# Optimization experiments

Measured on AMD Instinct MI355X. Metric: run time of the kernel, lower is better.

The kernel has to match this reference:

```python
import jax, jax.numpy as jnp
import numpy as np

B, S, D = 2, 2048, 2048          # batch, seq_len, model_dim
H, HD, RD, L = 16, 128, 64, 512  # heads, head_dim, rope_dim, latent_dim


def _rope_cos_sin(seq_len, dim, dtype):
    inv_freq = 1.0 / (10000.0 ** (jnp.arange(0, dim, 2, dtype=jnp.float32) / dim))
    freqs = jnp.outer(jnp.arange(seq_len, dtype=jnp.float32), inv_freq)  # [S, dim/2]
    emb = jnp.concatenate([freqs, freqs], axis=-1)                        # [S, dim]
    return jnp.cos(emb).astype(dtype), jnp.sin(emb).astype(dtype)


def _rotate_half(x):
    x1, x2 = jnp.split(x, 2, axis=-1)
    return jnp.concatenate([-x2, x1], axis=-1)


def _apply_rope(q, k):
    # q, k: [B, S, H, rope_dim]
    cos, sin = _rope_cos_sin(q.shape[1], q.shape[-1], q.dtype)
    cos = cos[None, :, None, :]
    sin = sin[None, :, None, :]
    return q * cos + _rotate_half(q) * sin, k * cos + _rotate_half(k) * sin


def setup_inputs() -> dict:
    key = jax.random.key(0)
    ks = jax.random.split(key, 6)
    x = jax.random.normal(ks[0], (B, S, D), dtype=jnp.float32)
    mask = jnp.tril(jnp.ones((1, 1, S, S), dtype=jnp.bool_))  # causal
    s = lambda fan_in: 1.0 / np.sqrt(fan_in)
    w_kv_down = jax.random.normal(ks[1], (D, L), jnp.float32) * s(D)
    w_kv_up = jax.random.normal(ks[2], (L, H * (2 * HD + RD)), jnp.float32) * s(L)
    w_q_down = jax.random.normal(ks[3], (D, L), jnp.float32) * s(D)
    w_q_up = jax.random.normal(ks[4], (L, H * (HD + RD)), jnp.float32) * s(L)
    w_o = jax.random.normal(ks[5], (H * HD, D), jnp.float32) * s(H * HD)
    return dict(x=x, mask=mask, w_kv_down=w_kv_down, w_kv_up=w_kv_up,
                w_q_down=w_q_down, w_q_up=w_q_up, w_o=w_o)


def reference(x, mask, w_kv_down, w_kv_up, w_q_down, w_q_up, w_o):
    b, s, _ = x.shape
    # low-rank KV path
    kv_full = (x @ w_kv_down @ w_kv_up).reshape(b, s, H, 2 * HD + RD)
    k_content = kv_full[..., :HD]
    k_rope = kv_full[..., HD:HD + RD]
    v = kv_full[..., HD + RD:]                     # [b, s, H, HD]
    # low-rank Q path
    q_full = (x @ w_q_down @ w_q_up).reshape(b, s, H, HD + RD)
    q_content = q_full[..., :HD]
    q_rope = q_full[..., HD:]
    # partial RoPE on the rope slice only
    q_rope, k_rope = _apply_rope(q_rope, k_rope)
    q = jnp.concatenate([q_content, q_rope], axis=-1)  # [b, s, H, HD+RD]
    k = jnp.concatenate([k_content, k_rope], axis=-1)
    scale = 1.0 / np.sqrt(HD + RD)
    scores = jnp.einsum('bqhd,bkhd->bhqk', q, k) * scale
    scores = jnp.where(mask, scores, jnp.finfo(scores.dtype).min)
    attn = jax.nn.softmax(scores, axis=-1)          # dropout_p=0.0 -> identity
    context = jnp.einsum('bhqk,bkhd->bqhd', attn, v).reshape(b, s, H * HD)
    return context @ w_o
```

## Files before the change

### kernel.cpp

```cpp
#include <hip/hip_runtime.h>
#include <hip/hip_bf16.h>

#define B_ 2
#define S_ 2048
#define D_ 2048
#define H_ 16
#define HD_ 128
#define RD_ 64
#define L_ 512
#define BS_ (B_ * S_)
#define KVH 320
#define QH 192

typedef unsigned short u16;
typedef __bf16 bf16x8 __attribute__((ext_vector_type(8)));
typedef float f32x4 __attribute__((ext_vector_type(4)));
typedef float f32x16 __attribute__((ext_vector_type(16)));
typedef unsigned short us8 __attribute__((ext_vector_type(8)));
typedef unsigned short us4 __attribute__((ext_vector_type(4)));

#define MFMA16(A, B, C) __builtin_amdgcn_mfma_f32_16x16x32_bf16((A), (B), (C), 0, 0, 0)
#define MFMA32(A, B, C) __builtin_amdgcn_mfma_f32_32x32x16_bf16((A), (B), (C), 0, 0, 0)

__device__ __forceinline__ u16 f2bf(float f) {
    unsigned int u = __builtin_bit_cast(unsigned int, f);
    u += 0x7FFFu + ((u >> 16) & 1u);
    return (u16)(u >> 16);
}
__device__ __forceinline__ float bf2f(u16 u) {
    unsigned int x = ((unsigned int)u) << 16;
    return __builtin_bit_cast(float, x);
}
__device__ __forceinline__ void async16(const void* g, void* l) {
    __builtin_amdgcn_global_load_lds((void __attribute__((address_space(1)))*)g,
                                     (void __attribute__((address_space(3)))*)l, 16, 0, 0);
}
__device__ __forceinline__ int swz4(int row) { return (row + (row >> 2)) & 3; }
__device__ __forceinline__ unsigned int cvtpk_bf16(float lo, float hi) {
    unsigned int r;
    asm("v_cvt_pk_bf16_f32 %0, %1, %2" : "=v"(r) : "v"(lo), "v"(hi));
    return r;
}

__global__ __launch_bounds__(256) void conv_f32_bf16(const float* __restrict__ in,
                                                     u16* __restrict__ outp) {
    const int i = blockIdx.x * 256 + threadIdx.x;
    float4 v = *(const float4*)(in + (size_t)i * 4);
    us4 o; o[0] = f2bf(v.x); o[1] = f2bf(v.y); o[2] = f2bf(v.z); o[3] = f2bf(v.w);
    *(us4*)(outp + (size_t)i * 4) = o;
}

__global__ __launch_bounds__(256) void transpose_f32_bf16(const float* __restrict__ W,
                                                          u16* __restrict__ Wt,
                                                          int K, int N) {
    __shared__ float tile[32][33];
    const int t = threadIdx.x, tx = t & 31, ty = t >> 5;
    const int n0 = blockIdx.x * 32, k0 = blockIdx.y * 32;
#pragma unroll
    for (int r = 0; r < 4; r++)
        tile[ty + 8 * r][tx] = W[(size_t)(k0 + ty + 8 * r) * N + n0 + tx];
    __syncthreads();
#pragma unroll
    for (int r = 0; r < 4; r++)
        Wt[(size_t)(n0 + ty + 8 * r) * K + k0 + tx] = f2bf(tile[tx][ty + 8 * r]);
}

__global__ __launch_bounds__(256) void transpose_v(const u16* __restrict__ kvf,
                                                   u16* __restrict__ vtg) {
    __shared__ u16 tile[32][33];
    const int t = threadIdx.x, tx = t & 31, ty = t >> 5;
    const int bh = blockIdx.z, b = bh >> 4, h = bh & 15;
    const int s0 = blockIdx.x * 32, d0 = blockIdx.y * 32;
#pragma unroll
    for (int r = 0; r < 4; r++)
        tile[ty + 8 * r][tx] = kvf[(size_t)(b * S_ + s0 + ty + 8 * r) * (H_ * KVH) + h * KVH + QH + d0 + tx];
    __syncthreads();
#pragma unroll
    for (int r = 0; r < 4; r++)
        vtg[((size_t)bh * HD_ + d0 + ty + 8 * r) * S_ + s0 + tx] = tile[tx][ty + 8 * r];
}

__global__ __launch_bounds__(256) void rope_both(u16* __restrict__ qf,
                                                 u16* __restrict__ kvf) {
    const int idx = blockIdx.x * 256 + threadIdx.x;
    const int d = idx & 31;
    const int h = (idx >> 5) & (H_ - 1);
    const int s = (idx >> 9) & (S_ - 1);
    const int b = idx >> 20;
    const int stride = blockIdx.y ? KVH : QH;
    u16* buf = blockIdx.y ? kvf : qf;

    const float inv_freq = powf(10000.0f, -(float)d * (1.0f / 32.0f));
    const float ang = (float)s * inv_freq;
    const float c = cosf(ang), sn = sinf(ang);

    u16* p = buf + ((size_t)((b * S_ + s) * H_) + h) * stride + HD_ + d;
    const float x1 = bf2f(p[0]);
    const float x2 = bf2f(p[32]);
    p[0]  = f2bf(x1 * c - x2 * sn);
    p[32] = f2bf(x2 * c + x1 * sn);
}

template <int WM, int WN, int TM, int TN, bool OUT_F32>
__global__ __launch_bounds__(WM * WN * 64) void gemm_bf16(
    const u16* __restrict__ A, int lda,
    const u16* __restrict__ Bt, int ldb,
    void* __restrict__ Cv, int ldc, int K) {
    constexpr int BMt = WM * TM * 16;
    constexpr int BNt = WN * TN * 16;
    constexpr int NW  = WM * WN;
    constexpr int CA  = BMt / 16;
    constexpr int CB  = BNt / 16;

    __shared__ u16 As[BMt * 32];
    __shared__ u16 Bs[BNt * 32];

    const int t = threadIdx.x, w = t >> 6, l = t & 63;
    const int quad = l >> 4, n16 = l & 15;
    const int wr = w / WN, wc = w % WN;
    const size_t m0 = (size_t)blockIdx.y * BMt;
    const size_t n0 = (size_t)blockIdx.x * BNt;
    const int rowc = l >> 2, sbp = l & 3;

    f32x4 acc[TM][TN];
#pragma unroll
    for (int i = 0; i < TM; i++)
#pragma unroll
        for (int j = 0; j < TN; j++) acc[i][j] = (f32x4){0.f, 0.f, 0.f, 0.f};

    for (int k0 = 0; k0 < K; k0 += 32) {
#pragma unroll
        for (int c = w; c < CA; c += NW) {
            const int row = c * 16 + rowc;
            const int colc = ((sbp - swz4(row)) & 3) * 8;
            async16(A + (m0 + row) * lda + k0 + colc, &As[c * 512 + l * 8]);
        }
#pragma unroll
        for (int c = w; c < CB; c += NW) {
            const int row = c * 16 + rowc;
            const int colc = ((sbp - swz4(row)) & 3) * 8;
            async16(Bt + (n0 + row) * ldb + k0 + colc, &Bs[c * 512 + l * 8]);
        }
        __syncthreads();

        bf16x8 af[TM], bfr[TN];
#pragma unroll
        for (int i = 0; i < TM; i++) {
            const int row = wr * TM * 16 + i * 16 + n16;
            af[i] = *(const bf16x8*)&As[row * 32 + ((quad + swz4(row)) & 3) * 8];
        }
#pragma unroll
        for (int j = 0; j < TN; j++) {
            const int row = wc * TN * 16 + j * 16 + n16;
            bfr[j] = *(const bf16x8*)&Bs[row * 32 + ((quad + swz4(row)) & 3) * 8];
        }
#pragma unroll
        for (int i = 0; i < TM; i++)
#pragma unroll
            for (int j = 0; j < TN; j++) acc[i][j] = MFMA16(af[i], bfr[j], acc[i][j]);
        __syncthreads();
    }

#pragma unroll
    for (int i = 0; i < TM; i++) {
#pragma unroll
        for (int j = 0; j < TN; j++) {
#pragma unroll
            for (int r = 0; r < 4; r++) {
                const size_t row = m0 + wr * TM * 16 + i * 16 + quad * 4 + r;
                const size_t col = n0 + wc * TN * 16 + j * 16 + n16;
                if (OUT_F32) ((float*)Cv)[row * ldc + col] = acc[i][j][r];
                else         ((u16*)Cv)[row * ldc + col] = f2bf(acc[i][j][r]);
            }
        }
    }
}

__global__ __launch_bounds__(256, 2) void attn_mfma(const u16* __restrict__ qf,
                                                    const u16* __restrict__ kvf,
                                                    const u16* __restrict__ vtg,
                                                    u16* __restrict__ ctx) {
    __shared__ u16 Ks[2][3 * 64 * 64];
    __shared__ u16 Vs[128 * 64];

    const int t = threadIdx.x, w = t >> 6, lane = t & 63;
    const int l31 = lane & 31, hi = lane >> 5;

    const int wg = blockIdx.x;
    const int xcd = wg & 7, ii = wg >> 3;
    const int tt = ii & 15;
    const int pp = (tt & 1) ? (tt >> 1) : (15 - (tt >> 1));
    const int qi = (ii & 32) ? (15 - pp) : pp;
    const int bh = xcd + 8 * (ii >> 4);
    const int b = bh >> 4, h = bh & 15;
    const int Q0 = qi * 128;

    const float sc2 = 1.442695041f / 13.856406461f;

    const u16* Kbase = kvf + (size_t)(b * S_) * (H_ * KVH) + h * KVH;
    const u16* Vbase = vtg + (size_t)bh * HD_ * S_;

    const int scol = ((lane & 7) ^ (lane >> 3)) * 8;
    const int krl  = lane >> 3;

    bf16x8 qfrag[12];
    {
        const u16* qr = qf + (size_t)(b * S_ + Q0 + w * 32 + l31) * (H_ * QH) + h * QH + hi * 8;
#pragma unroll
        for (int c = 0; c < 12; c++) qfrag[c] = *(const bf16x8*)(qr + c * 16);
    }
    asm volatile("" ::: "memory");

    f32x16 O[4];
#pragma unroll
    for (int i = 0; i < 4; i++)
#pragma unroll
        for (int r = 0; r < 16; r++) O[i][r] = 0.f;
    float lrun = 0.f;

    const int qg = Q0 + w * 32 + l31;
    const int qmaxw = Q0 + w * 32 + 31;
    const int nkt = Q0 / 64 + 2;

#define ISSUE_K(KT, BUF)                                                        \
    _Pragma("unroll")                                                           \
    for (int ch = w; ch < 24; ch += 4) {                                        \
        const int c3 = ch >> 3, kq = ch & 7;                                    \
        async16(Kbase + (size_t)((KT) * 64 + kq * 8 + krl) * (H_ * KVH)         \
                      + c3 * 64 + scol,                                         \
                &Ks[BUF][c3 * 4096 + kq * 512 + lane * 8]);                     \
    }
#define ISSUE_V(KT)                                                             \
    _Pragma("unroll")                                                           \
    for (int ch = w; ch < 16; ch += 4) {                                        \
        async16(Vbase + (size_t)(ch * 8 + krl) * S_ + (KT) * 64 + scol,         \
                &Vs[ch * 512 + lane * 8]);                                      \
    }

    ISSUE_K(0, 0);
    ISSUE_V(0);

    for (int kt = 0; kt < nkt; kt++) {
        const int cur = kt & 1;
        if (kt > 0) {
            asm volatile("s_barrier" ::: "memory");
            ISSUE_V(kt);
        }
        if (kt + 1 < nkt) {
            ISSUE_K(kt + 1, cur ^ 1);
            asm volatile("s_waitcnt vmcnt(10)" ::: "memory");
        } else {
            asm volatile("s_waitcnt vmcnt(4)" ::: "memory");
        }
        asm volatile("s_barrier" ::: "memory");

        const bool active = (kt * 64) <= qmaxw;
        bf16x8 pfrag[4];
        if (active) {
            const int swz = (l31 & 7) * 8;
            f32x16 sA, sB;
#pragma unroll
            for (int r = 0; r < 16; r++) { sA[r] = 0.f; sB[r] = 0.f; }
            __builtin_amdgcn_s_setprio(1);
#pragma unroll
            for (int c = 0; c < 12; c++) {
                const int cb = (c & 3) * 16 + hi * 8;
                const int base = (c >> 2) * 4096 + (cb ^ swz);
                bf16x8 kf0 = *(const bf16x8*)&Ks[cur][base + l31 * 64];
                bf16x8 kf1 = *(const bf16x8*)&Ks[cur][base + (32 + l31) * 64];
                sA = MFMA32(kf0, qfrag[c], sA);
                sB = MFMA32(kf1, qfrag[c], sB);
            }
            __builtin_amdgcn_s_setprio(0);

            const bool diag = (kt * 64 + 63) > (Q0 + w * 32);
#pragma unroll
            for (int r = 0; r < 16; r++) {
                const int crow = (r & 3) + 8 * (r >> 2) + 4 * hi;
                float pa = exp2f(sA[r] * sc2);
                float pb = exp2f(sB[r] * sc2);
                if (diag) {
                    if (kt * 64 + crow > qg) pa = 0.f;
                    if (kt * 64 + 32 + crow > qg) pb = 0.f;
                }
                lrun += pa + pb;
                sA[r] = pa;
                sB[r] = pb;
            }

#pragma unroll
            for (int s = 0; s < 4; s++) {
                const f32x16 src = (s < 2) ? sA : sB;
                const int r0 = (s & 1) * 8;
                unsigned int x0 = cvtpk_bf16(src[r0 + 0], src[r0 + 1]);
                unsigned int y0 = cvtpk_bf16(src[r0 + 4], src[r0 + 5]);
                unsigned int x1 = cvtpk_bf16(src[r0 + 2], src[r0 + 3]);
                unsigned int y1 = cvtpk_bf16(src[r0 + 6], src[r0 + 7]);
                asm volatile("v_permlane32_swap_b32 %0, %1" : "+v"(x0), "+v"(y0));
                asm volatile("v_permlane32_swap_b32 %0, %1" : "+v"(x1), "+v"(y1));
                union { unsigned int wv[4]; bf16x8 v; } u;
                u.wv[0] = x0; u.wv[1] = x1; u.wv[2] = y0; u.wv[3] = y1;
                pfrag[s] = u.v;
            }
        }

        if (kt + 1 < nkt) asm volatile("s_waitcnt vmcnt(6)" ::: "memory");
        else              asm volatile("s_waitcnt vmcnt(0)" ::: "memory");
        asm volatile("s_barrier" ::: "memory");

        if (active) {
            __builtin_amdgcn_s_setprio(1);
#pragma unroll
            for (int s = 0; s < 4; s++) {
#pragma unroll
                for (int dt = 0; dt < 4; dt++) {
                    const int d = dt * 32 + l31;
                    bf16x8 vf = *(const bf16x8*)&Vs[d * 64 + ((s * 16 + hi * 8) ^ ((d & 7) * 8))];
                    O[dt] = MFMA32(pfrag[s], vf, O[dt]);
                }
            }
            __builtin_amdgcn_s_setprio(0);
        }
    }
#undef ISSUE_K
#undef ISSUE_V

    lrun += __shfl_xor(lrun, 32, 64);
    float inv[16];
#pragma unroll
    for (int r = 0; r < 16; r++) {
        const int crow = (r & 3) + 8 * (r >> 2) + 4 * hi;
        inv[r] = 1.0f / __shfl(lrun, crow, 64);
    }
#pragma unroll
    for (int dt = 0; dt < 4; dt++)
#pragma unroll
        for (int r = 0; r < 16; r++) {
            const int crow = (r & 3) + 8 * (r >> 2) + 4 * hi;
            const int qrow = Q0 + w * 32 + crow;
            ctx[(size_t)(b * S_ + qrow) * (H_ * HD_) + h * HD_ + dt * 32 + l31] =
                f2bf(O[dt][r] * inv[r]);
        }
}

extern "C" void kernel_launch(void* const* d_in, const int* in_sizes, int n_in,
                              void* d_out, int out_size, void* d_ws, size_t ws_size,
                              hipStream_t stream) {
    const float* x         = (const float*)d_in[0];
    const float* w_kv_down = (const float*)d_in[2];
    const float* w_kv_up   = (const float*)d_in[3];
    const float* w_q_down  = (const float*)d_in[4];
    const float* w_q_up    = (const float*)d_in[5];
    const float* w_o       = (const float*)d_in[6];
    float* out = (float*)d_out;

    char* ws = (char*)d_ws;
    size_t off = 0;
    u16* xb      = (u16*)(ws + off); off += (size_t)BS_ * D_ * 2;
    u16* wdt     = (u16*)(ws + off); off += (size_t)1024 * D_ * 2;
    u16* wkvup_t = (u16*)(ws + off); off += (size_t)(H_ * KVH) * L_ * 2;
    u16* wqup_t  = (u16*)(ws + off); off += (size_t)(H_ * QH) * L_ * 2;
    u16* wo_t    = (u16*)(ws + off); off += (size_t)D_ * (H_ * HD_) * 2;
    u16* low     = (u16*)(ws + off); off += (size_t)BS_ * 1024 * 2;
    u16* kv_full = (u16*)(ws + off); off += (size_t)BS_ * H_ * KVH * 2;
    u16* q_full  = (u16*)(ws + off); off += (size_t)BS_ * H_ * QH * 2;
    u16* vtg     = (u16*)(ws + off); off += (size_t)B_ * H_ * HD_ * S_ * 2;
    u16* ctx     = (u16*)(ws + off); off += (size_t)BS_ * H_ * HD_ * 2;

    conv_f32_bf16<<<(BS_ * D_) / 1024, 256, 0, stream>>>(x, xb);
    transpose_f32_bf16<<<dim3(L_ / 32, D_ / 32), 256, 0, stream>>>(w_kv_down, wdt, D_, L_);
    transpose_f32_bf16<<<dim3(L_ / 32, D_ / 32), 256, 0, stream>>>(w_q_down, wdt + (size_t)512 * D_, D_, L_);
    transpose_f32_bf16<<<dim3((H_ * KVH) / 32, L_ / 32), 256, 0, stream>>>(w_kv_up, wkvup_t, L_, H_ * KVH);
    transpose_f32_bf16<<<dim3((H_ * QH) / 32, L_ / 32), 256, 0, stream>>>(w_q_up, wqup_t, L_, H_ * QH);
    transpose_f32_bf16<<<dim3(D_ / 32, (H_ * HD_) / 32), 256, 0, stream>>>(w_o, wo_t, H_ * HD_, D_);

    gemm_bf16<2, 2, 4, 2, false><<<dim3(1024 / 64, BS_ / 128), 256, 0, stream>>>(
        xb, D_, wdt, D_, low, 1024, D_);
    gemm_bf16<2, 2, 4, 4, false><<<dim3((H_ * KVH) / 128, BS_ / 128), 256, 0, stream>>>(
        low, 1024, wkvup_t, L_, kv_full, H_ * KVH, L_);
    gemm_bf16<2, 2, 4, 4, false><<<dim3((H_ * QH) / 128, BS_ / 128), 256, 0, stream>>>(
        low + 512, 1024, wqup_t, L_, q_full, H_ * QH, L_);

    rope_both<<<dim3((B_ * S_ * H_ * 32) / 256, 2), 256, 0, stream>>>(q_full, kv_full);

    transpose_v<<<dim3(S_ / 32, HD_ / 32, B_ * H_), 256, 0, stream>>>(kv_full, vtg);

    attn_mfma<<<dim3(512), 256, 0, stream>>>(q_full, kv_full, vtg, ctx);

    gemm_bf16<2, 2, 4, 4, true><<<dim3(D_ / 128, BS_ / 128), 256, 0, stream>>>(
        ctx, D_, wo_t, D_, out, D_, D_);
}
```

Measured before the change: 399.3 us.

## Software-pipeline attention QK and softmax-PV across tiles, pair causal query blocks per workgroup

The attention kernel is restructured so the QK^T MFMAs for the next key tile overlap the exp/PV work of the previous tile, using a triple-buffered V tile in LDS and precomputed swizzled LDS offsets. Each workgroup now processes a complementary pair of query blocks (qi and 15-qi) sequentially, giving it a constant amount of causal work, so the grid is halved and occupancy is set to one block per CU. The softmax scale times log2(e) is folded into the Q-projection GEMM epilogue through a new alpha parameter, which removes the per-element multiply in attention. The trade-offs are more LDS and register pressure, fewer resident waves, and Q being rounded to bf16 after scaling.

```diff
diff --git a/kernel.cpp b/kernel.cpp
--- a/kernel.cpp
+++ b/kernel.cpp
@@ -105,7 +105,7 @@
 __global__ __launch_bounds__(WM * WN * 64) void gemm_bf16(
     const u16* __restrict__ A, int lda,
     const u16* __restrict__ Bt, int ldb,
-    void* __restrict__ Cv, int ldc, int K) {
+    void* __restrict__ Cv, int ldc, int K, float alpha) {
     constexpr int BMt = WM * TM * 16;
     constexpr int BNt = WN * TN * 16;
     constexpr int NW  = WM * WN;
@@ -169,33 +169,29 @@
             for (int r = 0; r < 4; r++) {
                 const size_t row = m0 + wr * TM * 16 + i * 16 + quad * 4 + r;
                 const size_t col = n0 + wc * TN * 16 + j * 16 + n16;
-                if (OUT_F32) ((float*)Cv)[row * ldc + col] = acc[i][j][r];
-                else         ((u16*)Cv)[row * ldc + col] = f2bf(acc[i][j][r]);
+                const float v = acc[i][j][r] * alpha;
+                if (OUT_F32) ((float*)Cv)[row * ldc + col] = v;
+                else         ((u16*)Cv)[row * ldc + col] = f2bf(v);
             }
         }
     }
 }
 
-__global__ __launch_bounds__(256, 2) void attn_mfma(const u16* __restrict__ qf,
+__global__ __launch_bounds__(256, 1) void attn_mfma(const u16* __restrict__ qf,
                                                     const u16* __restrict__ kvf,
                                                     const u16* __restrict__ vtg,
                                                     u16* __restrict__ ctx) {
     __shared__ u16 Ks[2][3 * 64 * 64];
-    __shared__ u16 Vs[128 * 64];
+    __shared__ u16 Vs[3][128 * 64];
 
     const int t = threadIdx.x, w = t >> 6, lane = t & 63;
     const int l31 = lane & 31, hi = lane >> 5;
 
     const int wg = blockIdx.x;
-    const int xcd = wg & 7, ii = wg >> 3;
-    const int tt = ii & 15;
-    const int pp = (tt & 1) ? (tt >> 1) : (15 - (tt >> 1));
-    const int qi = (ii & 32) ? (15 - pp) : pp;
-    const int bh = xcd + 8 * (ii >> 4);
+    const int xcd = wg & 7, j = wg >> 3;
+    const int bh = xcd + 8 * (j & 3);
+    const int qpair = j >> 2;
     const int b = bh >> 4, h = bh & 15;
-    const int Q0 = qi * 128;
-
-    const float sc2 = 1.442695041f / 13.856406461f;
 
     const u16* Kbase = kvf + (size_t)(b * S_) * (H_ * KVH) + h * KVH;
     const u16* Vbase = vtg + (size_t)bh * HD_ * S_;
@@ -203,24 +199,16 @@
     const int scol = ((lane & 7) ^ (lane >> 3)) * 8;
     const int krl  = lane >> 3;
 
-    bf16x8 qfrag[12];
-    {
-        const u16* qr = qf + (size_t)(b * S_ + Q0 + w * 32 + l31) * (H_ * QH) + h * QH + hi * 8;
-#pragma unroll
-        for (int c = 0; c < 12; c++) qfrag[c] = *(const bf16x8*)(qr + c * 16);
-    }
-    asm volatile("" ::: "memory");
-
-    f32x16 O[4];
-#pragma unroll
-    for (int i = 0; i < 4; i++)
-#pragma unroll
-        for (int r = 0; r < 16; r++) O[i][r] = 0.f;
-    float lrun = 0.f;
-
-    const int qg = Q0 + w * 32 + l31;
-    const int qmaxw = Q0 + w * 32 + 31;
-    const int nkt = Q0 / 64 + 2;
+    int koff[12];
+#pragma unroll
+    for (int c = 0; c < 12; c++)
+        koff[c] = (c >> 2) * 4096 + (((c & 3) * 16 + hi * 8) ^ ((l31 & 7) * 8));
+    int voff[4][4];
+#pragma unroll
+    for (int s = 0; s < 4; s++)
+#pragma unroll
+        for (int dt = 0; dt < 4; dt++)
+            voff[s][dt] = (dt * 32 + l31) * 64 + ((s * 16 + hi * 8) ^ ((l31 & 7) * 8));
 
 #define ISSUE_K(KT, BUF)                                                        \
     _Pragma("unroll")                                                           \
@@ -230,117 +218,147 @@
                       + c3 * 64 + scol,                                         \
                 &Ks[BUF][c3 * 4096 + kq * 512 + lane * 8]);                     \
     }
-#define ISSUE_V(KT)                                                             \
+#define ISSUE_V(KT, VB)                                                         \
     _Pragma("unroll")                                                           \
     for (int ch = w; ch < 16; ch += 4) {                                        \
         async16(Vbase + (size_t)(ch * 8 + krl) * S_ + (KT) * 64 + scol,         \
-                &Vs[ch * 512 + lane * 8]);                                      \
-    }
-
-    ISSUE_K(0, 0);
-    ISSUE_V(0);
-
-    for (int kt = 0; kt < nkt; kt++) {
-        const int cur = kt & 1;
-        if (kt > 0) {
+                &Vs[VB][ch * 512 + lane * 8]);                                  \
+    }
+
+#define QK_TILE(TILE, SA, SB)                                                   \
+    {                                                                           \
+        const int kb_ = (TILE) & 1;                                             \
+        _Pragma("unroll")                                                       \
+        for (int r = 0; r < 16; r++) { SA[r] = 0.f; SB[r] = 0.f; }              \
+        _Pragma("unroll")                                                       \
+        for (int c = 0; c < 12; c++) {                                          \
+            bf16x8 kf0 = *(const bf16x8*)&Ks[kb_][koff[c] + l31 * 64];          \
+            bf16x8 kf1 = *(const bf16x8*)&Ks[kb_][koff[c] + (32 + l31) * 64];   \
+            SA = MFMA32(kf0, qfrag[c], SA);                                     \
+            SB = MFMA32(kf1, qfrag[c], SB);                                     \
+        }                                                                       \
+    }
+
+#define SMPV_TILE(TILE, SA, SB)                                                 \
+    {                                                                           \
+        const int vb_ = (TILE) % 3;                                             \
+        const bool diag_ = ((TILE) * 64 + 63) > (Q0 + w * 32);                  \
+        _Pragma("unroll")                                                       \
+        for (int r = 0; r < 16; r++) {                                          \
+            float pa = exp2f(SA[r]);                                            \
+            float pb = exp2f(SB[r]);                                            \
+            if (diag_) {                                                        \
+                const int crow_ = (r & 3) + 8 * (r >> 2) + 4 * hi;              \
+                if ((TILE) * 64 + crow_ > qg) pa = 0.f;                         \
+                if ((TILE) * 64 + 32 + crow_ > qg) pb = 0.f;                    \
+            }                                                                   \
+            lrun += pa + pb;                                                    \
+            SA[r] = pa; SB[r] = pb;                                             \
+        }                                                                       \
+        bf16x8 pfrag[4];                                                        \
+        _Pragma("unroll")                                                       \
+        for (int s = 0; s < 4; s++) {                                           \
+            const int r0 = (s & 1) * 8;                                         \
+            unsigned int x0, y0, x1, y1;                                        \
+            if (s < 2) {                                                        \
+                x0 = cvtpk_bf16(SA[r0 + 0], SA[r0 + 1]);                        \
+                y0 = cvtpk_bf16(SA[r0 + 4], SA[r0 + 5]);                        \
+                x1 = cvtpk_bf16(SA[r0 + 2], SA[r0 + 3]);                        \
+                y1 = cvtpk_bf16(SA[r0 + 6], SA[r0 + 7]);                        \
+            } else {                                                            \
+                x0 = cvtpk_bf16(SB[r0 + 0], SB[r0 + 1]);                        \
+                y0 = cvtpk_bf16(SB[r0 + 4], SB[r0 + 5]);                        \
+                x1 = cvtpk_bf16(SB[r0 + 2], SB[r0 + 3]);                        \
+                y1 = cvtpk_bf16(SB[r0 + 6], SB[r0 + 7]);                        \
+            }                                                                   \
+            asm volatile("v_permlane32_swap_b32 %0, %1" : "+v"(x0), "+v"(y0));  \
+            asm volatile("v_permlane32_swap_b32 %0, %1" : "+v"(x1), "+v"(y1));  \
+            union { unsigned int wv[4]; bf16x8 v; } u_;                         \
+            u_.wv[0] = x0; u_.wv[1] = x1; u_.wv[2] = y0; u_.wv[3] = y1;         \
+            pfrag[s] = u_.v;                                                    \
+        }                                                                       \
+        _Pragma("unroll")                                                       \
+        for (int s = 0; s < 4; s++) {                                           \
+            _Pragma("unroll")                                                   \
+            for (int dt = 0; dt < 4; dt++) {                                    \
+                bf16x8 vf = *(const bf16x8*)&Vs[vb_][voff[s][dt]];              \
+                O[dt] = MFMA32(pfrag[s], vf, O[dt]);                            \
+            }                                                                   \
+        }                                                                       \
+    }
+
+#pragma unroll 1
+    for (int half = 0; half < 2; half++) {
+        const int qi = half ? (15 - qpair) : qpair;
+        const int Q0 = qi * 128;
+        const int nkt = 2 * qi + 2;
+        const int qmaxw = Q0 + w * 32 + 31;
+        const int qg = Q0 + w * 32 + l31;
+
+        asm volatile("s_barrier" ::: "memory");
+
+        bf16x8 qfrag[12];
+        {
+            const u16* qr = qf + (size_t)(b * S_ + Q0 + w * 32 + l31) * (H_ * QH) + h * QH + hi * 8;
+#pragma unroll
+            for (int c = 0; c < 12; c++) qfrag[c] = *(const bf16x8*)(qr + c * 16);
+        }
+        asm volatile("" ::: "memory");
+
+        f32x16 O[4];
+#pragma unroll
+        for (int i = 0; i < 4; i++)
+#pragma unroll
+            for (int r = 0; r < 16; r++) O[i][r] = 0.f;
+        float lrun = 0.f;
+        f32x16 sEa, sEb, sOa, sOb;
+
+        ISSUE_K(0, 0);
+        ISSUE_V(0, 0);
+
+        for (int kt = 0; kt < nkt; kt += 2) {
+            ISSUE_K(kt + 1, (kt + 1) & 1);
+            ISSUE_V(kt + 1, (kt + 1) % 3);
+            asm volatile("s_waitcnt vmcnt(10)" ::: "memory");
             asm volatile("s_barrier" ::: "memory");
-            ISSUE_V(kt);
-        }
-        if (kt + 1 < nkt) {
-            ISSUE_K(kt + 1, cur ^ 1);
-            asm volatile("s_waitcnt vmcnt(10)" ::: "memory");
-        } else {
-            asm volatile("s_waitcnt vmcnt(4)" ::: "memory");
-        }
-        asm volatile("s_barrier" ::: "memory");
-
-        const bool active = (kt * 64) <= qmaxw;
-        bf16x8 pfrag[4];
-        if (active) {
-            const int swz = (l31 & 7) * 8;
-            f32x16 sA, sB;
-#pragma unroll
-            for (int r = 0; r < 16; r++) { sA[r] = 0.f; sB[r] = 0.f; }
-            __builtin_amdgcn_s_setprio(1);
-#pragma unroll
-            for (int c = 0; c < 12; c++) {
-                const int cb = (c & 3) * 16 + hi * 8;
-                const int base = (c >> 2) * 4096 + (cb ^ swz);
-                bf16x8 kf0 = *(const bf16x8*)&Ks[cur][base + l31 * 64];
-                bf16x8 kf1 = *(const bf16x8*)&Ks[cur][base + (32 + l31) * 64];
-                sA = MFMA32(kf0, qfrag[c], sA);
-                sB = MFMA32(kf1, qfrag[c], sB);
+            QK_TILE(kt, sEa, sEb);
+            if (kt > 0) SMPV_TILE(kt - 1, sOa, sOb);
+            asm volatile("s_barrier" ::: "memory");
+            if (kt + 2 < nkt) {
+                ISSUE_K(kt + 2, kt & 1);
+                ISSUE_V(kt + 2, (kt + 2) % 3);
+                asm volatile("s_waitcnt vmcnt(10)" ::: "memory");
+            } else {
+                asm volatile("s_waitcnt vmcnt(0)" ::: "memory");
             }
-            __builtin_amdgcn_s_setprio(0);
-
-            const bool diag = (kt * 64 + 63) > (Q0 + w * 32);
+            asm volatile("s_barrier" ::: "memory");
+            if ((kt + 1) * 64 <= qmaxw) QK_TILE(kt + 1, sOa, sOb);
+            SMPV_TILE(kt, sEa, sEb);
+            asm volatile("s_barrier" ::: "memory");
+        }
+        if ((nkt - 1) * 64 <= qmaxw) SMPV_TILE(nkt - 1, sOa, sOb);
+
+        lrun += __shfl_xor(lrun, 32, 64);
+        float inv_[16];
+#pragma unroll
+        for (int r = 0; r < 16; r++) {
+            const int crow = (r & 3) + 8 * (r >> 2) + 4 * hi;
+            inv_[r] = 1.0f / __shfl(lrun, crow, 64);
+        }
+#pragma unroll
+        for (int dt = 0; dt < 4; dt++)
 #pragma unroll
             for (int r = 0; r < 16; r++) {
                 const int crow = (r & 3) + 8 * (r >> 2) + 4 * hi;
-                float pa = exp2f(sA[r] * sc2);
-                float pb = exp2f(sB[r] * sc2);
-                if (diag) {
-                    if (kt * 64 + crow > qg) pa = 0.f;
-                    if (kt * 64 + 32 + crow > qg) pb = 0.f;
-                }
-                lrun += pa + pb;
-                sA[r] = pa;
-                sB[r] = pb;
+                const int qrow = Q0 + w * 32 + crow;
+                ctx[(size_t)(b * S_ + qrow) * (H_ * HD_) + h * HD_ + dt * 32 + l31] =
+                    f2bf(O[dt][r] * inv_[r]);
             }
-
-#pragma unroll
-            for (int s = 0; s < 4; s++) {
-                const f32x16 src = (s < 2) ? sA : sB;
-                const int r0 = (s & 1) * 8;
-                unsigned int x0 = cvtpk_bf16(src[r0 + 0], src[r0 + 1]);
-                unsigned int y0 = cvtpk_bf16(src[r0 + 4], src[r0 + 5]);
-                unsigned int x1 = cvtpk_bf16(src[r0 + 2], src[r0 + 3]);
-                unsigned int y1 = cvtpk_bf16(src[r0 + 6], src[r0 + 7]);
-                asm volatile("v_permlane32_swap_b32 %0, %1" : "+v"(x0), "+v"(y0));
-                asm volatile("v_permlane32_swap_b32 %0, %1" : "+v"(x1), "+v"(y1));
-                union { unsigned int wv[4]; bf16x8 v; } u;
-                u.wv[0] = x0; u.wv[1] = x1; u.wv[2] = y0; u.wv[3] = y1;
-                pfrag[s] = u.v;
-            }
-        }
-
-        if (kt + 1 < nkt) asm volatile("s_waitcnt vmcnt(6)" ::: "memory");
-        else              asm volatile("s_waitcnt vmcnt(0)" ::: "memory");
-        asm volatile("s_barrier" ::: "memory");
-
-        if (active) {
-            __builtin_amdgcn_s_setprio(1);
-#pragma unroll
-            for (int s = 0; s < 4; s++) {
-#pragma unroll
-                for (int dt = 0; dt < 4; dt++) {
-                    const int d = dt * 32 + l31;
-                    bf16x8 vf = *(const bf16x8*)&Vs[d * 64 + ((s * 16 + hi * 8) ^ ((d & 7) * 8))];
-                    O[dt] = MFMA32(pfrag[s], vf, O[dt]);
-                }
-            }
-            __builtin_amdgcn_s_setprio(0);
-        }
     }
 #undef ISSUE_K
 #undef ISSUE_V
-
-    lrun += __shfl_xor(lrun, 32, 64);
-    float inv[16];
-#pragma unroll
-    for (int r = 0; r < 16; r++) {
-        const int crow = (r & 3) + 8 * (r >> 2) + 4 * hi;
-        inv[r] = 1.0f / __shfl(lrun, crow, 64);
-    }
-#pragma unroll
-    for (int dt = 0; dt < 4; dt++)
-#pragma unroll
-        for (int r = 0; r < 16; r++) {
-            const int crow = (r & 3) + 8 * (r >> 2) + 4 * hi;
-            const int qrow = Q0 + w * 32 + crow;
-            ctx[(size_t)(b * S_ + qrow) * (H_ * HD_) + h * HD_ + dt * 32 + l31] =
-                f2bf(O[dt][r] * inv[r]);
-        }
+#undef QK_TILE
+#undef SMPV_TILE
 }
 
 extern "C" void kernel_launch(void* const* d_in, const int* in_sizes, int n_in,
@@ -367,6 +385,8 @@
     u16* vtg     = (u16*)(ws + off); off += (size_t)B_ * H_ * HD_ * S_ * 2;
     u16* ctx     = (u16*)(ws + off); off += (size_t)BS_ * H_ * HD_ * 2;
 
+    const float qscale = 1.442695041f / 13.856406461f;
+
     conv_f32_bf16<<<(BS_ * D_) / 1024, 256, 0, stream>>>(x, xb);
     transpose_f32_bf16<<<dim3(L_ / 32, D_ / 32), 256, 0, stream>>>(w_kv_down, wdt, D_, L_);
     transpose_f32_bf16<<<dim3(L_ / 32, D_ / 32), 256, 0, stream>>>(w_q_down, wdt + (size_t)512 * D_, D_, L_);
@@ -375,18 +395,18 @@
     transpose_f32_bf16<<<dim3(D_ / 32, (H_ * HD_) / 32), 256, 0, stream>>>(w_o, wo_t, H_ * HD_, D_);
 
     gemm_bf16<2, 2, 4, 2, false><<<dim3(1024 / 64, BS_ / 128), 256, 0, stream>>>(
-        xb, D_, wdt, D_, low, 1024, D_);
+        xb, D_, wdt, D_, low, 1024, D_, 1.0f);
     gemm_bf16<2, 2, 4, 4, false><<<dim3((H_ * KVH) / 128, BS_ / 128), 256, 0, stream>>>(
-        low, 1024, wkvup_t, L_, kv_full, H_ * KVH, L_);
+        low, 1024, wkvup_t, L_, kv_full, H_ * KVH, L_, 1.0f);
     gemm_bf16<2, 2, 4, 4, false><<<dim3((H_ * QH) / 128, BS_ / 128), 256, 0, stream>>>(
-        low + 512, 1024, wqup_t, L_, q_full, H_ * QH, L_);
+        low + 512, 1024, wqup_t, L_, q_full, H_ * QH, L_, qscale);
 
     rope_both<<<dim3((B_ * S_ * H_ * 32) / 256, 2), 256, 0, stream>>>(q_full, kv_full);
 
     transpose_v<<<dim3(S_ / 32, HD_ / 32, B_ * H_), 256, 0, stream>>>(kv_full, vtg);
 
-    attn_mfma<<<dim3(512), 256, 0, stream>>>(q_full, kv_full, vtg, ctx);
+    attn_mfma<<<dim3(256), 256, 0, stream>>>(q_full, kv_full, vtg, ctx);
 
     gemm_bf16<2, 2, 4, 4, true><<<dim3(D_ / 128, BS_ / 128), 256, 0, stream>>>(
-        ctx, D_, wo_t, D_, out, D_, D_);
-}
+        ctx, D_, wo_t, D_, out, D_, D_, 1.0f);
+}
```

Result: slower. 411.9 us (+3.2%).

## Shrink attention tiles to 64 queries and 32-key steps, fold softmax scale into Q GEMM

Applied to the files above, without the earlier changes.

Attention blocks now process 64 query rows with 2 waves (128 threads) and step through keys 32 at a time, launching 1024 blocks in a longest-first order instead of 512 blocks with a paired-tile schedule. LDS offsets for K and V fragments are precomputed, and the V tile layout and swizzle are changed to match the narrower tile. The softmax scale times log2(e) moves into the Q up-projection GEMM epilogue through a new alpha parameter, which removes a multiply per score. The aim is better load balance across the causal triangle and more blocks per CU. The cost is less K/V reuse per block, more barriers per key, and applying RoPE to already-scaled bf16 Q values.

```diff
diff --git a/kernel.cpp b/kernel.cpp
--- a/kernel.cpp
+++ b/kernel.cpp
@@ -105,7 +105,7 @@
 __global__ __launch_bounds__(WM * WN * 64) void gemm_bf16(
     const u16* __restrict__ A, int lda,
     const u16* __restrict__ Bt, int ldb,
-    void* __restrict__ Cv, int ldc, int K) {
+    void* __restrict__ Cv, int ldc, int K, float alpha) {
     constexpr int BMt = WM * TM * 16;
     constexpr int BNt = WN * TN * 16;
     constexpr int NW  = WM * WN;
@@ -169,39 +169,49 @@
             for (int r = 0; r < 4; r++) {
                 const size_t row = m0 + wr * TM * 16 + i * 16 + quad * 4 + r;
                 const size_t col = n0 + wc * TN * 16 + j * 16 + n16;
-                if (OUT_F32) ((float*)Cv)[row * ldc + col] = acc[i][j][r];
-                else         ((u16*)Cv)[row * ldc + col] = f2bf(acc[i][j][r]);
-            }
-        }
-    }
-}
-
-__global__ __launch_bounds__(256, 2) void attn_mfma(const u16* __restrict__ qf,
+                const float v = acc[i][j][r] * alpha;
+                if (OUT_F32) ((float*)Cv)[row * ldc + col] = v;
+                else         ((u16*)Cv)[row * ldc + col] = f2bf(v);
+            }
+        }
+    }
+}
+
+__global__ __launch_bounds__(128, 2) void attn_mfma(const u16* __restrict__ qf,
                                                     const u16* __restrict__ kvf,
                                                     const u16* __restrict__ vtg,
                                                     u16* __restrict__ ctx) {
-    __shared__ u16 Ks[2][3 * 64 * 64];
-    __shared__ u16 Vs[128 * 64];
+    __shared__ u16 Ks[2][3 * 32 * 64];
+    __shared__ u16 Vs[128 * 32];
 
     const int t = threadIdx.x, w = t >> 6, lane = t & 63;
     const int l31 = lane & 31, hi = lane >> 5;
 
     const int wg = blockIdx.x;
-    const int xcd = wg & 7, ii = wg >> 3;
-    const int tt = ii & 15;
-    const int pp = (tt & 1) ? (tt >> 1) : (15 - (tt >> 1));
-    const int qi = (ii & 32) ? (15 - pp) : pp;
-    const int bh = xcd + 8 * (ii >> 4);
+    const int xcd = wg & 7, j = wg >> 3;
+    const int bh = xcd + 8 * (j & 3);
+    const int qt = 31 - (j >> 2);
     const int b = bh >> 4, h = bh & 15;
-    const int Q0 = qi * 128;
-
-    const float sc2 = 1.442695041f / 13.856406461f;
+    const int Q0 = qt * 64;
 
     const u16* Kbase = kvf + (size_t)(b * S_) * (H_ * KVH) + h * KVH;
     const u16* Vbase = vtg + (size_t)bh * HD_ * S_;
 
     const int scol = ((lane & 7) ^ (lane >> 3)) * 8;
     const int krl  = lane >> 3;
+    const int vrow = lane >> 2;
+    const int vcol = ((lane & 3) ^ (vrow & 3)) * 8;
+
+    int koff[12];
+#pragma unroll
+    for (int c = 0; c < 12; c++)
+        koff[c] = (c >> 2) * 2048 + (((c & 3) * 16 + hi * 8) ^ ((l31 & 7) * 8));
+    int voff[2][4];
+#pragma unroll
+    for (int s = 0; s < 2; s++)
+#pragma unroll
+        for (int dt = 0; dt < 4; dt++)
+            voff[s][dt] = (dt * 32 + l31) * 32 + ((s * 16 + hi * 8) ^ ((l31 & 3) * 8));
 
     bf16x8 qfrag[12];
     {
@@ -220,20 +230,20 @@
 
     const int qg = Q0 + w * 32 + l31;
     const int qmaxw = Q0 + w * 32 + 31;
-    const int nkt = Q0 / 64 + 2;
+    const int nkt = 2 * qt + 2;
 
 #define ISSUE_K(KT, BUF)                                                        \
     _Pragma("unroll")                                                           \
-    for (int ch = w; ch < 24; ch += 4) {                                        \
-        const int c3 = ch >> 3, kq = ch & 7;                                    \
-        async16(Kbase + (size_t)((KT) * 64 + kq * 8 + krl) * (H_ * KVH)         \
+    for (int ch = w; ch < 12; ch += 2) {                                        \
+        const int c3 = ch >> 2, kq = ch & 3;                                    \
+        async16(Kbase + (size_t)((KT) * 32 + kq * 8 + krl) * (H_ * KVH)         \
                       + c3 * 64 + scol,                                         \
-                &Ks[BUF][c3 * 4096 + kq * 512 + lane * 8]);                     \
+                &Ks[BUF][c3 * 2048 + kq * 512 + lane * 8]);                     \
     }
 #define ISSUE_V(KT)                                                             \
     _Pragma("unroll")                                                           \
-    for (int ch = w; ch < 16; ch += 4) {                                        \
-        async16(Vbase + (size_t)(ch * 8 + krl) * S_ + (KT) * 64 + scol,         \
+    for (int ch = w; ch < 8; ch += 2) {                                         \
+        async16(Vbase + (size_t)(ch * 16 + vrow) * S_ + (KT) * 32 + vcol,       \
                 &Vs[ch * 512 + lane * 8]);                                      \
     }
 
@@ -254,53 +264,42 @@
         }
         asm volatile("s_barrier" ::: "memory");
 
-        const bool active = (kt * 64) <= qmaxw;
-        bf16x8 pfrag[4];
+        const bool active = (kt * 32) <= qmaxw;
+        bf16x8 pfrag[2];
         if (active) {
-            const int swz = (l31 & 7) * 8;
-            f32x16 sA, sB;
-#pragma unroll
-            for (int r = 0; r < 16; r++) { sA[r] = 0.f; sB[r] = 0.f; }
+            f32x16 sA;
+#pragma unroll
+            for (int r = 0; r < 16; r++) sA[r] = 0.f;
             __builtin_amdgcn_s_setprio(1);
 #pragma unroll
             for (int c = 0; c < 12; c++) {
-                const int cb = (c & 3) * 16 + hi * 8;
-                const int base = (c >> 2) * 4096 + (cb ^ swz);
-                bf16x8 kf0 = *(const bf16x8*)&Ks[cur][base + l31 * 64];
-                bf16x8 kf1 = *(const bf16x8*)&Ks[cur][base + (32 + l31) * 64];
-                sA = MFMA32(kf0, qfrag[c], sA);
-                sB = MFMA32(kf1, qfrag[c], sB);
+                bf16x8 kf = *(const bf16x8*)&Ks[cur][koff[c] + l31 * 64];
+                sA = MFMA32(kf, qfrag[c], sA);
             }
             __builtin_amdgcn_s_setprio(0);
 
-            const bool diag = (kt * 64 + 63) > (Q0 + w * 32);
+            const bool diag = (kt * 32 + 31) > (Q0 + w * 32);
 #pragma unroll
             for (int r = 0; r < 16; r++) {
                 const int crow = (r & 3) + 8 * (r >> 2) + 4 * hi;
-                float pa = exp2f(sA[r] * sc2);
-                float pb = exp2f(sB[r] * sc2);
-                if (diag) {
-                    if (kt * 64 + crow > qg) pa = 0.f;
-                    if (kt * 64 + 32 + crow > qg) pb = 0.f;
-                }
-                lrun += pa + pb;
+                float pa = exp2f(sA[r]);
+                if (diag && (kt * 32 + crow > qg)) pa = 0.f;
+                lrun += pa;
                 sA[r] = pa;
-                sB[r] = pb;
-            }
-
-#pragma unroll
-            for (int s = 0; s < 4; s++) {
-                const f32x16 src = (s < 2) ? sA : sB;
-                const int r0 = (s & 1) * 8;
-                unsigned int x0 = cvtpk_bf16(src[r0 + 0], src[r0 + 1]);
-                unsigned int y0 = cvtpk_bf16(src[r0 + 4], src[r0 + 5]);
-                unsigned int x1 = cvtpk_bf16(src[r0 + 2], src[r0 + 3]);
-                unsigned int y1 = cvtpk_bf16(src[r0 + 6], src[r0 + 7]);
+            }
+
+#pragma unroll
+            for (int s = 0; s < 2; s++) {
+                const int r0 = s * 8;
+                unsigned int x0 = cvtpk_bf16(sA[r0 + 0], sA[r0 + 1]);
+                unsigned int y0 = cvtpk_bf16(sA[r0 + 4], sA[r0 + 5]);
+                unsigned int x1 = cvtpk_bf16(sA[r0 + 2], sA[r0 + 3]);
+                unsigned int y1 = cvtpk_bf16(sA[r0 + 6], sA[r0 + 7]);
                 asm volatile("v_permlane32_swap_b32 %0, %1" : "+v"(x0), "+v"(y0));
                 asm volatile("v_permlane32_swap_b32 %0, %1" : "+v"(x1), "+v"(y1));
-                union { unsigned int wv[4]; bf16x8 v; } u;
-                u.wv[0] = x0; u.wv[1] = x1; u.wv[2] = y0; u.wv[3] = y1;
-                pfrag[s] = u.v;
+                union { unsigned int wv[4]; bf16x8 v; } u_;
+                u_.wv[0] = x0; u_.wv[1] = x1; u_.wv[2] = y0; u_.wv[3] = y1;
+                pfrag[s] = u_.v;
             }
         }
 
@@ -311,11 +310,10 @@
         if (active) {
             __builtin_amdgcn_s_setprio(1);
 #pragma unroll
-            for (int s = 0; s < 4; s++) {
+            for (int s = 0; s < 2; s++) {
 #pragma unroll
                 for (int dt = 0; dt < 4; dt++) {
-                    const int d = dt * 32 + l31;
-                    bf16x8 vf = *(const bf16x8*)&Vs[d * 64 + ((s * 16 + hi * 8) ^ ((d & 7) * 8))];
+                    bf16x8 vf = *(const bf16x8*)&Vs[voff[s][dt]];
                     O[dt] = MFMA32(pfrag[s], vf, O[dt]);
                 }
             }
@@ -326,11 +324,11 @@
 #undef ISSUE_V
 
     lrun += __shfl_xor(lrun, 32, 64);
-    float inv[16];
+    float inv_[16];
 #pragma unroll
     for (int r = 0; r < 16; r++) {
         const int crow = (r & 3) + 8 * (r >> 2) + 4 * hi;
-        inv[r] = 1.0f / __shfl(lrun, crow, 64);
+        inv_[r] = 1.0f / __shfl(lrun, crow, 64);
     }
 #pragma unroll
     for (int dt = 0; dt < 4; dt++)
@@ -339,7 +337,7 @@
             const int crow = (r & 3) + 8 * (r >> 2) + 4 * hi;
             const int qrow = Q0 + w * 32 + crow;
             ctx[(size_t)(b * S_ + qrow) * (H_ * HD_) + h * HD_ + dt * 32 + l31] =
-                f2bf(O[dt][r] * inv[r]);
+                f2bf(O[dt][r] * inv_[r]);
         }
 }
 
@@ -367,6 +365,8 @@
     u16* vtg     = (u16*)(ws + off); off += (size_t)B_ * H_ * HD_ * S_ * 2;
     u16* ctx     = (u16*)(ws + off); off += (size_t)BS_ * H_ * HD_ * 2;
 
+    const float qscale = 1.442695041f / 13.856406461f;
+
     conv_f32_bf16<<<(BS_ * D_) / 1024, 256, 0, stream>>>(x, xb);
     transpose_f32_bf16<<<dim3(L_ / 32, D_ / 32), 256, 0, stream>>>(w_kv_down, wdt, D_, L_);
     transpose_f32_bf16<<<dim3(L_ / 32, D_ / 32), 256, 0, stream>>>(w_q_down, wdt + (size_t)512 * D_, D_, L_);
@@ -375,18 +375,18 @@
     transpose_f32_bf16<<<dim3(D_ / 32, (H_ * HD_) / 32), 256, 0, stream>>>(w_o, wo_t, H_ * HD_, D_);
 
     gemm_bf16<2, 2, 4, 2, false><<<dim3(1024 / 64, BS_ / 128), 256, 0, stream>>>(
-        xb, D_, wdt, D_, low, 1024, D_);
+        xb, D_, wdt, D_, low, 1024, D_, 1.0f);
     gemm_bf16<2, 2, 4, 4, false><<<dim3((H_ * KVH) / 128, BS_ / 128), 256, 0, stream>>>(
-        low, 1024, wkvup_t, L_, kv_full, H_ * KVH, L_);
+        low, 1024, wkvup_t, L_, kv_full, H_ * KVH, L_, 1.0f);
     gemm_bf16<2, 2, 4, 4, false><<<dim3((H_ * QH) / 128, BS_ / 128), 256, 0, stream>>>(
-        low + 512, 1024, wqup_t, L_, q_full, H_ * QH, L_);
+        low + 512, 1024, wqup_t, L_, q_full, H_ * QH, L_, qscale);
 
     rope_both<<<dim3((B_ * S_ * H_ * 32) / 256, 2), 256, 0, stream>>>(q_full, kv_full);
 
     transpose_v<<<dim3(S_ / 32, HD_ / 32, B_ * H_), 256, 0, stream>>>(kv_full, vtg);
 
-    attn_mfma<<<dim3(512), 256, 0, stream>>>(q_full, kv_full, vtg, ctx);
+    attn_mfma<<<dim3(1024), 128, 0, stream>>>(q_full, kv_full, vtg, ctx);
 
     gemm_bf16<2, 2, 4, 4, true><<<dim3(D_ / 128, BS_ / 128), 256, 0, stream>>>(
-        ctx, D_, wo_t, D_, out, D_, D_);
-}
+        ctx, D_, wo_t, D_, out, D_, D_, 1.0f);
+}
```

After: 416.6 us. 4.3% more time.

## Fold softmax scale into Q projection, precompute RoPE table, vectorize V transpose

Applied to the files above, without the earlier changes.

The softmax scale times log2(e) moves into the epilogue of the Q up-projection GEMM through a new alpha parameter, which removes a multiply per score inside the attention inner loop. RoPE cos/sin values are computed once into a small table instead of calling powf/sinf/cosf per element. The V transpose now uses 64x64 tiles with 16-byte vector loads and stores. The trade-off is that Q is rounded to bf16 after scaling, which changes numerics slightly, and there is one extra kernel launch for the table.

```diff
diff --git a/kernel.cpp b/kernel.cpp
--- a/kernel.cpp
+++ b/kernel.cpp
@@ -67,21 +67,37 @@
 
 __global__ __launch_bounds__(256) void transpose_v(const u16* __restrict__ kvf,
                                                    u16* __restrict__ vtg) {
-    __shared__ u16 tile[32][33];
-    const int t = threadIdx.x, tx = t & 31, ty = t >> 5;
+    __shared__ u16 tile[64][72];
+    const int t = threadIdx.x;
+    const int r = t >> 2, cb = (t & 3) * 16;
     const int bh = blockIdx.z, b = bh >> 4, h = bh & 15;
-    const int s0 = blockIdx.x * 32, d0 = blockIdx.y * 32;
-#pragma unroll
-    for (int r = 0; r < 4; r++)
-        tile[ty + 8 * r][tx] = kvf[(size_t)(b * S_ + s0 + ty + 8 * r) * (H_ * KVH) + h * KVH + QH + d0 + tx];
+    const int s0 = blockIdx.x * 64, d0 = blockIdx.y * 64;
+
+    const u16* src = kvf + (size_t)(b * S_ + s0 + r) * (H_ * KVH) + h * KVH + QH + d0 + cb;
+    *(us8*)&tile[r][cb]     = *(const us8*)(src);
+    *(us8*)&tile[r][cb + 8] = *(const us8*)(src + 8);
     __syncthreads();
-#pragma unroll
-    for (int r = 0; r < 4; r++)
-        vtg[((size_t)bh * HD_ + d0 + ty + 8 * r) * S_ + s0 + tx] = tile[tx][ty + 8 * r];
+
+    u16 tmp[16];
+#pragma unroll
+    for (int j = 0; j < 16; j++) tmp[j] = tile[cb + j][r];
+    u16* dst = vtg + ((size_t)bh * HD_ + d0 + r) * S_ + s0 + cb;
+    *(us8*)(dst)     = *(us8*)&tmp[0];
+    *(us8*)(dst + 8) = *(us8*)&tmp[8];
+}
+
+__global__ __launch_bounds__(256) void rope_table(float* __restrict__ cs) {
+    const int idx = blockIdx.x * 256 + threadIdx.x;
+    const int d = idx & 31, s = idx >> 5;
+    const float inv_freq = powf(10000.0f, -(float)d * (1.0f / 32.0f));
+    const float ang = (float)s * inv_freq;
+    cs[s * 64 + d]      = cosf(ang);
+    cs[s * 64 + 32 + d] = sinf(ang);
 }
 
 __global__ __launch_bounds__(256) void rope_both(u16* __restrict__ qf,
-                                                 u16* __restrict__ kvf) {
+                                                 u16* __restrict__ kvf,
+                                                 const float* __restrict__ cs) {
     const int idx = blockIdx.x * 256 + threadIdx.x;
     const int d = idx & 31;
     const int h = (idx >> 5) & (H_ - 1);
@@ -90,9 +106,8 @@
     const int stride = blockIdx.y ? KVH : QH;
     u16* buf = blockIdx.y ? kvf : qf;
 
-    const float inv_freq = powf(10000.0f, -(float)d * (1.0f / 32.0f));
-    const float ang = (float)s * inv_freq;
-    const float c = cosf(ang), sn = sinf(ang);
+    const float c  = cs[s * 64 + d];
+    const float sn = cs[s * 64 + 32 + d];
 
     u16* p = buf + ((size_t)((b * S_ + s) * H_) + h) * stride + HD_ + d;
     const float x1 = bf2f(p[0]);
@@ -105,7 +120,7 @@
 __global__ __launch_bounds__(WM * WN * 64) void gemm_bf16(
     const u16* __restrict__ A, int lda,
     const u16* __restrict__ Bt, int ldb,
-    void* __restrict__ Cv, int ldc, int K) {
+    void* __restrict__ Cv, int ldc, int K, float alpha) {
     constexpr int BMt = WM * TM * 16;
     constexpr int BNt = WN * TN * 16;
     constexpr int NW  = WM * WN;
@@ -169,8 +184,9 @@
             for (int r = 0; r < 4; r++) {
                 const size_t row = m0 + wr * TM * 16 + i * 16 + quad * 4 + r;
                 const size_t col = n0 + wc * TN * 16 + j * 16 + n16;
-                if (OUT_F32) ((float*)Cv)[row * ldc + col] = acc[i][j][r];
-                else         ((u16*)Cv)[row * ldc + col] = f2bf(acc[i][j][r]);
+                const float v = acc[i][j][r] * alpha;
+                if (OUT_F32) ((float*)Cv)[row * ldc + col] = v;
+                else         ((u16*)Cv)[row * ldc + col] = f2bf(v);
             }
         }
     }
@@ -194,8 +210,6 @@
     const int bh = xcd + 8 * (ii >> 4);
     const int b = bh >> 4, h = bh & 15;
     const int Q0 = qi * 128;
-
-    const float sc2 = 1.442695041f / 13.856406461f;
 
     const u16* Kbase = kvf + (size_t)(b * S_) * (H_ * KVH) + h * KVH;
     const u16* Vbase = vtg + (size_t)bh * HD_ * S_;
@@ -277,8 +291,8 @@
 #pragma unroll
             for (int r = 0; r < 16; r++) {
                 const int crow = (r & 3) + 8 * (r >> 2) + 4 * hi;
-                float pa = exp2f(sA[r] * sc2);
-                float pb = exp2f(sB[r] * sc2);
+                float pa = exp2f(sA[r]);
+                float pb = exp2f(sB[r]);
                 if (diag) {
                     if (kt * 64 + crow > qg) pa = 0.f;
                     if (kt * 64 + 32 + crow > qg) pb = 0.f;
@@ -366,7 +380,11 @@
     u16* q_full  = (u16*)(ws + off); off += (size_t)BS_ * H_ * QH * 2;
     u16* vtg     = (u16*)(ws + off); off += (size_t)B_ * H_ * HD_ * S_ * 2;
     u16* ctx     = (u16*)(ws + off); off += (size_t)BS_ * H_ * HD_ * 2;
-
+    float* ropecs = (float*)(ws + off); off += (size_t)S_ * 64 * 4;
+
+    const float qscale = 1.442695041f / 13.856406461f;
+
+    rope_table<<<256, 256, 0, stream>>>(ropecs);
     conv_f32_bf16<<<(BS_ * D_) / 1024, 256, 0, stream>>>(x, xb);
     transpose_f32_bf16<<<dim3(L_ / 32, D_ / 32), 256, 0, stream>>>(w_kv_down, wdt, D_, L_);
     transpose_f32_bf16<<<dim3(L_ / 32, D_ / 32), 256, 0, stream>>>(w_q_down, wdt + (size_t)512 * D_, D_, L_);
@@ -375,18 +393,18 @@
     transpose_f32_bf16<<<dim3(D_ / 32, (H_ * HD_) / 32), 256, 0, stream>>>(w_o, wo_t, H_ * HD_, D_);
 
     gemm_bf16<2, 2, 4, 2, false><<<dim3(1024 / 64, BS_ / 128), 256, 0, stream>>>(
-        xb, D_, wdt, D_, low, 1024, D_);
+        xb, D_, wdt, D_, low, 1024, D_, 1.0f);
     gemm_bf16<2, 2, 4, 4, false><<<dim3((H_ * KVH) / 128, BS_ / 128), 256, 0, stream>>>(
-        low, 1024, wkvup_t, L_, kv_full, H_ * KVH, L_);
+        low, 1024, wkvup_t, L_, kv_full, H_ * KVH, L_, 1.0f);
     gemm_bf16<2, 2, 4, 4, false><<<dim3((H_ * QH) / 128, BS_ / 128), 256, 0, stream>>>(
-        low + 512, 1024, wqup_t, L_, q_full, H_ * QH, L_);
-
-    rope_both<<<dim3((B_ * S_ * H_ * 32) / 256, 2), 256, 0, stream>>>(q_full, kv_full);
-
-    transpose_v<<<dim3(S_ / 32, HD_ / 32, B_ * H_), 256, 0, stream>>>(kv_full, vtg);
+        low + 512, 1024, wqup_t, L_, q_full, H_ * QH, L_, qscale);
+
+    rope_both<<<dim3((B_ * S_ * H_ * 32) / 256, 2), 256, 0, stream>>>(q_full, kv_full, ropecs);
+
+    transpose_v<<<dim3(S_ / 64, HD_ / 64, B_ * H_), 256, 0, stream>>>(kv_full, vtg);
 
     attn_mfma<<<dim3(512), 256, 0, stream>>>(q_full, kv_full, vtg, ctx);
 
     gemm_bf16<2, 2, 4, 4, true><<<dim3(D_ / 128, BS_ / 128), 256, 0, stream>>>(
-        ctx, D_, wo_t, D_, out, D_, D_);
-}
+        ctx, D_, wo_t, D_, out, D_, D_, 1.0f);
+}
```

Measured after the change: 390.4 us. 2.2% less time.
